# Kernel tuning notes

Hardware: AMD Instinct MI355X
Metric: run time of the kernel (lower is better)

The kernel has to match this reference:

```python
import jax, jax.numpy as jnp
import numpy as np

B, F, H, W = 1, 4, 20, 44
P = H * W            # 880 tokens per frame (20*44, from max_attention_size = 15*880)
S = F * P            # 3520 packed tokens
DIM, NH, FFN, OUT = 1536, 12, 6144, 64   # OUT = prod(patch_size)*out_dim = 4*16
HD = DIM // NH       # 128
C = HD // 2          # 64 rotary complex pairs
EPS = 1e-6


def _rope_angles():
    # Wan 3D RoPE: split C pairs as (C-2*(C//3), C//3, C//3) over (frame, h, w)
    cf, ch, cw = C - 2 * (C // 3), C // 3, C // 3
    def tab(n, cp):
        inv = 1.0 / (10000.0 ** (np.arange(cp) / cp))
        return np.outer(np.arange(n), inv)
    af = np.broadcast_to(tab(F, cf)[:, None, None, :], (F, H, W, cf))
    ah = np.broadcast_to(tab(H, ch)[None, :, None, :], (F, H, W, ch))
    aw = np.broadcast_to(tab(W, cw)[None, None, :, :], (F, H, W, cw))
    return np.concatenate([af, ah, aw], -1).reshape(S, C).astype(np.float32)


def setup_inputs() -> dict:
    key = jax.random.key(0)
    ks = jax.random.split(key, 24)
    g = lambda i, shape, s=0.02: jax.random.normal(ks[i], shape, dtype=jnp.float32) * s
    inp = {
        'x': jax.random.normal(ks[0], (B, S, DIM), dtype=jnp.float32),
        'e': g(1, (B, F, 6, DIM), 1.0),
        'e_head': g(2, (B, F, 2, DIM), 1.0),
        'rope_angles': jnp.asarray(_rope_angles()),
        'mod_block': g(3, (1, 6, DIM), 1.0 / float(np.sqrt(DIM))),
        'mod_head': g(4, (1, 2, DIM), 1.0 / float(np.sqrt(DIM))),
        'Wq': g(5, (DIM, DIM)), 'bq': jnp.zeros((DIM,), jnp.float32),
        'Wk': g(6, (DIM, DIM)), 'bk': jnp.zeros((DIM,), jnp.float32),
        'Wv': g(7, (DIM, DIM)), 'bv': jnp.zeros((DIM,), jnp.float32),
        'Wo': g(8, (DIM, DIM)), 'bo': jnp.zeros((DIM,), jnp.float32),
        'wq_norm': jnp.ones((DIM,), jnp.float32),
        'wk_norm': jnp.ones((DIM,), jnp.float32),
        'W1': g(9, (DIM, FFN)), 'b1': jnp.zeros((FFN,), jnp.float32),
        'W2': g(10, (FFN, DIM)), 'b2': jnp.zeros((DIM,), jnp.float32),
        'Wh': g(11, (DIM, OUT)), 'bh': jnp.zeros((OUT,), jnp.float32),
    }
    return inp


def _ln(x):
    # WanLayerNorm without elementwise affine
    m = jnp.mean(x, axis=-1, keepdims=True)
    v = jnp.var(x, axis=-1, keepdims=True)
    return (x - m) * jax.lax.rsqrt(v + EPS)


def _rms(x, w):
    return x * jax.lax.rsqrt(jnp.mean(x * x, axis=-1, keepdims=True) + EPS) * w


def _rope(t, ang):
    # t: [B,S,NH,HD]; adjacent pairs form complex numbers (view_as_complex style)
    tr = t.reshape(B, S, NH, C, 2)
    cos = jnp.cos(ang)[None, :, None, :]
    sin = jnp.sin(ang)[None, :, None, :]
    t0, t1 = tr[..., 0], tr[..., 1]
    return jnp.stack([t0 * cos - t1 * sin, t0 * sin + t1 * cos], -1).reshape(B, S, NH, HD)


def reference(x, e, e_head, rope_angles, mod_block, mod_head,
              Wq, bq, Wk, bk, Wv, bv, Wo, bo, wq_norm, wk_norm,
              W1, b1, W2, b2, Wh, bh):
    # ---- AdaLN modulation split (6-way) ----
    em = mod_block[:, None] + e                      # [B,F,6,DIM]
    e0, e1, e2, e3, e4, e5 = [em[:, :, i][:, :, None, :] for i in range(6)]

    xf = x.reshape(B, F, P, DIM)
    h = (_ln(xf) * (1 + e1) + e0).reshape(B, S, DIM)

    # ---- QK-RMSNorm + RoPE self attention (block-causal, block = one frame) ----
    q = _rope(_rms(h @ Wq + bq, wq_norm).reshape(B, S, NH, HD), rope_angles)
    k = _rope(_rms(h @ Wk + bk, wk_norm).reshape(B, S, NH, HD), rope_angles)
    v = (h @ Wv + bv).reshape(B, S, NH, HD)

    blk = jnp.arange(S) // P
    mask = blk[None, :] <= blk[:, None]              # [S,S] block-causal
    scores = jnp.einsum('bqhd,bkhd->bhqk', q, k) / np.float32(np.sqrt(HD))
    scores = jnp.where(mask[None, None], scores, jnp.float32(-1e30))
    attn = jax.nn.softmax(scores, axis=-1)
    y = jnp.einsum('bhqk,bkhd->bqhd', attn, v).reshape(B, S, DIM) @ Wo + bo

    xf = xf + y.reshape(B, F, P, DIM) * e2

    # ---- FFN with AdaLN modulation ----
    hf = (_ln(xf) * (1 + e4) + e3).reshape(B, S, DIM)
    ff = jax.nn.gelu(hf @ W1 + b1) @ W2 + b2
    xf = xf + ff.reshape(B, F, P, DIM) * e5

    # ---- OutputHead: modulated norm + linear ----
    eh = mod_head[:, None] + e_head                  # [B,F,2,DIM]
    eh0 = eh[:, :, 0][:, :, None, :]
    eh1 = eh[:, :, 1][:, :, None, :]
    out = (_ln(xf) * (1 + eh1) + eh0) @ Wh + bh      # [B,F,P,OUT]
    return out
```

## Files before the change

### kernel.cpp

```cpp
#include <hip/hip_runtime.h>
#include <cstdint>
#include <cstddef>

typedef __bf16 bf16;
typedef __bf16 bf16x2 __attribute__((ext_vector_type(2)));
typedef __bf16 bf16x4 __attribute__((ext_vector_type(4)));
typedef __bf16 bf16x8 __attribute__((ext_vector_type(8)));
typedef float f32x4 __attribute__((ext_vector_type(4)));
typedef unsigned int u32x4 __attribute__((ext_vector_type(4)));

#define S_TOK 3520
#define S_PAD 3584
#define P_TOK 880
#define NFRM 4
#define DIM 1536
#define NH 12
#define HD 128
#define FFN_D 6144
#define NOUT 64
#define EPSV 1e-6f
#define QSCALE 0.12751743f

__device__ __forceinline__ f32x4 mfma16(bf16x8 a, bf16x8 b, f32x4 c) {
  return __builtin_amdgcn_mfma_f32_16x16x32_bf16(a, b, c, 0, 0, 0);
}

__device__ __forceinline__ void gload_lds16(const bf16* g, bf16* l) {
  __builtin_amdgcn_global_load_lds(
      (const __attribute__((address_space(1))) unsigned int*)g,
      (__attribute__((address_space(3))) unsigned int*)l, 16, 0, 0);
}

__device__ __forceinline__ uint32_t pk2(float lo, float hi) {
  bf16x2 t;
  t[0] = (bf16)lo;
  t[1] = (bf16)hi;
  return __builtin_bit_cast(uint32_t, t);
}

__global__ __launch_bounds__(256) void k_prep(const float* __restrict__ e,
                                              const float* __restrict__ e_head,
                                              const float* __restrict__ mod_block,
                                              const float* __restrict__ mod_head,
                                              float* __restrict__ em,
                                              float* __restrict__ ehm) {
  int i = blockIdx.x * 256 + threadIdx.x;
  if (i < NFRM * 6 * DIM) em[i] = mod_block[i % (6 * DIM)] + e[i];
  int j = i - NFRM * 6 * DIM;
  if (j >= 0 && j < NFRM * 2 * DIM) ehm[j] = mod_head[j % (2 * DIM)] + e_head[j];
}

__global__ __launch_bounds__(256) void k_zero_vpad(bf16* __restrict__ vc) {
  size_t base = ((size_t)blockIdx.x * 28 + 27) * 4096 + 2048 + (size_t)threadIdx.x * 8;
#pragma unroll
  for (int i = 0; i < 8; ++i) vc[base + i] = (bf16)0.f;
}

__global__ __launch_bounds__(256) void k_transpose(const float* __restrict__ W,
                                                   bf16* __restrict__ Wt, int K, int N) {
  __shared__ float tile[32][33];
  int n0 = blockIdx.x * 32, k0 = blockIdx.y * 32;
  int tx = threadIdx.x & 31, ty = threadIdx.x >> 5;
#pragma unroll
  for (int j = 0; j < 4; ++j) {
    int k = k0 + ty * 4 + j;
    float v = (n0 + tx < N) ? W[(size_t)k * N + n0 + tx] : 0.f;
    tile[ty * 4 + j][tx] = v;
  }
  __syncthreads();
#pragma unroll
  for (int j = 0; j < 4; ++j) {
    int n = n0 + ty * 4 + j;
    if (n < N) Wt[(size_t)n * K + k0 + tx] = (bf16)tile[tx][ty * 4 + j];
  }
}

__global__ __launch_bounds__(256) void k_adaln(const float* __restrict__ in,
                                               bf16* __restrict__ out,
                                               const float* __restrict__ e_shift,
                                               const float* __restrict__ e_scale,
                                               int fstride) {
  int tok = blockIdx.x;
  int t = threadIdx.x;
  bf16* orow = out + (size_t)tok * DIM;
  if (tok >= S_TOK) {
#pragma unroll
    for (int i = 0; i < 6; ++i) orow[t * 6 + i] = (bf16)0.f;
    return;
  }
  const float* xrow = in + (size_t)tok * DIM;
  float v[6];
  float s = 0.f, sq = 0.f;
#pragma unroll
  for (int i = 0; i < 6; ++i) {
    v[i] = xrow[t * 6 + i];
    s += v[i];
    sq += v[i] * v[i];
  }
  for (int off = 32; off; off >>= 1) {
    s += __shfl_down(s, off);
    sq += __shfl_down(sq, off);
  }
  __shared__ float red[8];
  int wv = t >> 6, lane = t & 63;
  if (lane == 0) { red[wv] = s; red[4 + wv] = sq; }
  __syncthreads();
  float ts = red[0] + red[1] + red[2] + red[3];
  float tq = red[4] + red[5] + red[6] + red[7];
  float mean = ts * (1.f / DIM);
  float var = tq * (1.f / DIM) - mean * mean;
  float rstd = rsqrtf(var + EPSV);
  int f = tok / P_TOK;
  const float* sh = e_shift + (size_t)f * fstride;
  const float* sc = e_scale + (size_t)f * fstride;
#pragma unroll
  for (int i = 0; i < 6; ++i) {
    int d = t * 6 + i;
    orow[d] = (bf16)((v[i] - mean) * rstd * (1.f + sc[d]) + sh[d]);
  }
}

__global__ __launch_bounds__(256) void k_qkv_post(const bf16* __restrict__ qkv,
                                                  const float* __restrict__ wqn,
                                                  const float* __restrict__ wkn,
                                                  const float* __restrict__ ang,
                                                  bf16* __restrict__ qb,
                                                  bf16* __restrict__ kb,
                                                  bf16* __restrict__ vc) {
  int s = blockIdx.x;
  int t = threadIdx.x;
  const bf16* row = qkv + (size_t)s * 3 * DIM;
  float qv[6], kv[6], vv[6];
  float sqq = 0.f, sqk = 0.f;
  int d0 = t * 6;
#pragma unroll
  for (int i = 0; i < 6; ++i) {
    int d = d0 + i;
    qv[i] = (float)row[d];
    kv[i] = (float)row[DIM + d];
    vv[i] = (float)row[2 * DIM + d];
    sqq += qv[i] * qv[i];
    sqk += kv[i] * kv[i];
  }
  float a1 = sqq, a2 = sqk;
  for (int off = 32; off; off >>= 1) {
    a1 += __shfl_down(a1, off);
    a2 += __shfl_down(a2, off);
  }
  __shared__ float red[8];
  int wv = t >> 6, lane = t & 63;
  if (lane == 0) { red[wv] = a1; red[4 + wv] = a2; }
  __syncthreads();
  float tq = red[0] + red[1] + red[2] + red[3];
  float tk = red[4] + red[5] + red[6] + red[7];
  float rq = rsqrtf(tq * (1.f / DIM) + EPSV);
  float rk = rsqrtf(tk * (1.f / DIM) + EPSV);
#pragma unroll
  for (int p = 0; p < 3; ++p) {
    int d = d0 + p * 2;
    int h = d >> 7;
    int hd = d & 127;
    int c = hd >> 1;
    float a = ang[(size_t)s * 64 + c];
    float sa, ca;
    sincosf(a, &sa, &ca);
    float q0 = qv[p * 2] * rq * wqn[d], q1 = qv[p * 2 + 1] * rq * wqn[d + 1];
    float k0 = kv[p * 2] * rk * wkn[d], k1 = kv[p * 2 + 1] * rk * wkn[d + 1];
    size_t base = ((size_t)h * S_TOK + s) * HD + hd;
    qb[base]     = (bf16)((q0 * ca - q1 * sa) * QSCALE);
    qb[base + 1] = (bf16)((q0 * sa + q1 * ca) * QSCALE);
    kb[base]     = (bf16)(k0 * ca - k1 * sa);
    kb[base + 1] = (bf16)(k0 * sa + k1 * ca);
  }
  int f = s / P_TOK;
  int l = s - f * P_TOK;
  int lb = l >> 5, gg = (l >> 3) & 3, r = l & 7;
#pragma unroll
  for (int i = 0; i < 6; ++i) {
    int d = d0 + i;
    int h = d >> 7, hd = d & 127;
    vc[((((size_t)(h * NFRM + f)) * 28 + lb) * 512 + gg * 128 + hd) * 8 + r] = (bf16)vv[i];
  }
}

__global__ __launch_bounds__(320) void k_attn(const bf16* __restrict__ qb,
                                              const bf16* __restrict__ kb,
                                              const bf16* __restrict__ vc,
                                              bf16* __restrict__ parto,
                                              float* __restrict__ partml) {
  __shared__ __align__(16) bf16 Ks[2][512 * 8];
  __shared__ __align__(16) bf16 Vs[2][512 * 8];
  int h = blockIdx.x / 110;
  int p = blockIdx.x % 110;
  int f = (p < 11) ? 0 : (p < 33) ? 1 : (p < 66) ? 2 : 3;
  int cum = (f == 0) ? 0 : (f == 1) ? 11 : (f == 2) ? 33 : 66;
  int w = p - cum;
  int kc = w / 11;
  int qt = f * 11 + w % 11;
  int slot = blockIdx.x;
  int t = threadIdx.x;
  int wv = t >> 6, lane = t & 63;
  int r16 = lane & 15, g = lane >> 4;
  int q0 = qt * 80 + wv * 16;
  int kv0 = kc * P_TOK;
  const bf16* qbase = qb + ((size_t)h * S_TOK + q0 + r16) * HD + g * 8;
  bf16x8 qf[4];
#pragma unroll
  for (int kk = 0; kk < 4; ++kk) qf[kk] = *(const bf16x8*)(qbase + kk * 32);
  f32x4 acc[8] = {};
  float mrow = -1e30f, lrow = 0.f;
  int src01 = r16 + ((2 * g) & 3) * 16;
  int src23 = src01 + 16;
  bool glo = (g < 2);
  int sB = t + 256;
  int kr0 = t >> 4, kl0 = t & 15;
  int ks0 = (kl0 & 8) | ((kl0 ^ kr0) & 7);
  int kr1 = sB >> 4, kl1 = sB & 15;
  int ks1 = (kl1 & 8) | ((kl1 ^ kr1) & 7);
  const bf16* kh = kb + (size_t)h * S_TOK * HD;
  const bf16* vchunk = vc + ((size_t)(h * NFRM + kc)) * 28 * 4096;
#define STAGE_ATT(buf, jj)                                                  \
  do {                                                                      \
    int kvoj = (jj) * 32;                                                   \
    int gr0 = kv0 + kvoj + kr0; if (gr0 >= S_TOK) gr0 = 0;                  \
    int gr1 = kv0 + kvoj + kr1; if (gr1 >= S_TOK) gr1 = 0;                  \
    gload_lds16(kh + (size_t)gr0 * HD + ks0 * 8, Ks[buf] + t * 8);          \
    gload_lds16(kh + (size_t)gr1 * HD + ks1 * 8, Ks[buf] + sB * 8);         \
    gload_lds16(vchunk + (size_t)(jj) * 4096 + t * 8, Vs[buf] + t * 8);     \
    gload_lds16(vchunk + (size_t)(jj) * 4096 + sB * 8, Vs[buf] + sB * 8);   \
  } while (0)
  const int nsteps = (P_TOK + 31) >> 5;
  if (t < 256) STAGE_ATT(0, 0);
  int cur = 0;
  int vrb = g * 128 + r16;
  for (int j = 0; j < nsteps; ++j) {
    if (j + 1 < nsteps) {
      if (t < 256) STAGE_ATT(cur ^ 1, j + 1);
      asm volatile("s_waitcnt vmcnt(4)" ::: "memory");
    } else {
      asm volatile("s_waitcnt vmcnt(0)" ::: "memory");
    }
    __builtin_amdgcn_s_barrier();
    f32x4 st0 = {0.f, 0.f, 0.f, 0.f}, st1 = {0.f, 0.f, 0.f, 0.f};
#pragma unroll
    for (int kk = 0; kk < 4; ++kk) {
      int sl = g + 4 * kk;
      int ss = (sl & 8) | ((sl ^ r16) & 7);
      bf16x8 k0 = *(const bf16x8*)(Ks[cur] + (r16 * 16 + ss) * 8);
      bf16x8 k1 = *(const bf16x8*)(Ks[cur] + ((16 + r16) * 16 + ss) * 8);
      st0 = mfma16(k0, qf[kk], st0);
      st1 = mfma16(k1, qf[kk], st1);
    }
    float hm = (j == nsteps - 1) ? -1e30f : 0.f;
    float a0[4], a1[4];
#pragma unroll
    for (int r = 0; r < 4; ++r) {
      a0[r] = st0[r];
      a1[r] = st1[r] + hm;
    }
    float tm = fmaxf(fmaxf(fmaxf(a0[0], a0[1]), fmaxf(a0[2], a0[3])),
                     fmaxf(fmaxf(a1[0], a1[1]), fmaxf(a1[2], a1[3])));
    tm = fmaxf(tm, __shfl_xor(tm, 16));
    tm = fmaxf(tm, __shfl_xor(tm, 32));
    bool defer = __all(tm <= mrow + 8.f);
    if (!defer) {
      float mn = fmaxf(mrow, tm);
      float scl = exp2f(mrow - mn);
      lrow *= scl;
#pragma unroll
      for (int hb = 0; hb < 8; ++hb) {
        acc[hb][0] *= scl;
        acc[hb][1] *= scl;
        acc[hb][2] *= scl;
        acc[hb][3] *= scl;
      }
      mrow = mn;
    }
    float p0[4], p1[4], ps = 0.f;
#pragma unroll
    for (int r = 0; r < 4; ++r) {
      p0[r] = exp2f(a0[r] - mrow);
      p1[r] = exp2f(a1[r] - mrow);
      ps += p0[r] + p1[r];
    }
    lrow += ps;
    uint32_t A0 = pk2(p0[0], p0[1]), A1 = pk2(p0[2], p0[3]);
    uint32_t B0 = pk2(p1[0], p1[1]), B1 = pk2(p1[2], p1[3]);
    uint32_t sA0 = __shfl(A0, src01), sA1 = __shfl(A1, src01);
    uint32_t sB0 = __shfl(B0, src01), sB1 = __shfl(B1, src01);
    uint32_t tA0 = __shfl(A0, src23), tA1 = __shfl(A1, src23);
    uint32_t tB0 = __shfl(B0, src23), tB1 = __shfl(B1, src23);
    u32x4 wds;
    wds[0] = glo ? sA0 : sB0;
    wds[1] = glo ? sA1 : sB1;
    wds[2] = glo ? tA0 : tB0;
    wds[3] = glo ? tA1 : tB1;
    bf16x8 pb = __builtin_bit_cast(bf16x8, wds);
    const bf16* vsl = Vs[cur] + (size_t)vrb * 8;
#pragma unroll
    for (int hb = 0; hb < 8; ++hb) {
      bf16x8 vfr = *(const bf16x8*)(vsl + hb * 128);
      acc[hb] = mfma16(vfr, pb, acc[hb]);
    }
    asm volatile("" ::: "memory");
    __builtin_amdgcn_s_barrier();
    cur ^= 1;
  }
#undef STAGE_ATT
  lrow += __shfl_xor(lrow, 16);
  lrow += __shfl_xor(lrow, 32);
  bf16* obase = parto + ((size_t)slot * 5 + wv) * 2048;
#pragma unroll
  for (int hb = 0; hb < 8; ++hb) {
    bf16x4 ov;
    ov[0] = (bf16)acc[hb][0];
    ov[1] = (bf16)acc[hb][1];
    ov[2] = (bf16)acc[hb][2];
    ov[3] = (bf16)acc[hb][3];
    *(bf16x4*)(obase + (hb * 64 + lane) * 4) = ov;
  }
  if (g == 0) {
    float* mlb = partml + ((size_t)slot * 5 + wv) * 32;
    mlb[r16] = mrow;
    mlb[16 + r16] = lrow;
  }
}

__global__ __launch_bounds__(256) void k_att_reduce(const bf16* __restrict__ parto,
                                                    const float* __restrict__ partml,
                                                    bf16* __restrict__ attb) {
  int b = blockIdx.x;
  int h = b / 44, qt = b % 44;
  int f = qt / 11, j = qt % 11;
  int cum = (f == 0) ? 0 : (f == 1) ? 11 : (f == 2) ? 33 : 66;
  int t = threadIdx.x;
  int d = t & 127, half = t >> 7;
  int hb = d >> 4, g = (d >> 2) & 3, r = d & 3;
  int q0 = qt * 80;
  for (int it = 0; it < 40; ++it) {
    int qloc = it + 40 * half;
    int wv = qloc >> 4, r16 = qloc & 15;
    float m[4], l[4];
    float mt = -1e30f;
    for (int kc = 0; kc <= f; ++kc) {
      int slot = h * 110 + cum + kc * 11 + j;
      const float* mlb = partml + ((size_t)slot * 5 + wv) * 32;
      m[kc] = mlb[r16];
      l[kc] = mlb[16 + r16];
      mt = fmaxf(mt, m[kc]);
    }
    float lt = 0.f, o = 0.f;
    for (int kc = 0; kc <= f; ++kc) {
      int slot = h * 110 + cum + kc * 11 + j;
      float wgt = exp2f(m[kc] - mt);
      lt += l[kc] * wgt;
      o += (float)parto[(((size_t)slot * 5 + wv) * 8 + hb) * 256 + (g * 16 + r16) * 4 + r] * wgt;
    }
    attb[(size_t)(q0 + qloc) * DIM + h * HD + d] = (bf16)(o / lt);
  }
}

struct GemmP {
  const bf16* A;
  const bf16* Bt;
  int K;
  int Mtiles;
  int Ntiles;
  int Mreal;
  int mode;
  const float* bias0;
  const float* bias1;
  const float* bias2;
  const float* res;
  const float* emod;
  int e_fstride;
  float* outf;
  bf16* outb;
  int ldo;
};

__global__ __launch_bounds__(512, 4) void k_gemm(GemmP p) {
  int nwg = p.Mtiles * p.Ntiles;
  int bid = blockIdx.x;
  int xq = nwg >> 3, xr = nwg & 7;
  int xcd = bid & 7, jj = bid >> 3;
  int wg = (xcd < xr ? xcd * (xq + 1) : xr * (xq + 1) + (xcd - xr) * xq) + jj;
  int bm = wg % p.Mtiles;
  int bn = wg / p.Mtiles;
  __shared__ __align__(16) bf16 Asl[2][128 * 64];
  __shared__ __align__(16) bf16 Bsl[2][128 * 64];
  int t = threadIdx.x, lane = t & 63, wv = t >> 6;
  int r16 = lane & 15, g = lane >> 4;
  int s7 = r16 & 7;
  int wr = wv >> 2, wc = wv & 3;
  f32x4 acc[4][2] = {};
  const bf16* Ag = p.A + (size_t)bm * 128 * p.K;
  const bf16* Bg = p.Bt + (size_t)bn * 128 * p.K;
  int b0 = t, b1 = t + 512;
  int rw0 = b0 >> 3, cb0 = (b0 & 7) ^ (rw0 & 7);
  int rw1 = b1 >> 3, cb1 = (b1 & 7) ^ (rw1 & 7);
#define STAGE(d, kt)                                                          \
  do {                                                                        \
    int k0s = (kt) * 64;                                                      \
    gload_lds16(Ag + (size_t)rw0 * p.K + k0s + cb0 * 8, Asl[d] + b0 * 8);     \
    gload_lds16(Ag + (size_t)rw1 * p.K + k0s + cb1 * 8, Asl[d] + b1 * 8);     \
    gload_lds16(Bg + (size_t)rw0 * p.K + k0s + cb0 * 8, Bsl[d] + b0 * 8);     \
    gload_lds16(Bg + (size_t)rw1 * p.K + k0s + cb1 * 8, Bsl[d] + b1 * 8);     \
  } while (0)
  const int nt = p.K >> 6;
  STAGE(0, 0);
  int cur = 0;
  for (int tt = 0; tt < nt; ++tt) {
    if (tt + 1 < nt) {
      STAGE(cur ^ 1, tt + 1);
      asm volatile("s_waitcnt vmcnt(4)" ::: "memory");
    } else {
      asm volatile("s_waitcnt vmcnt(0)" ::: "memory");
    }
    __builtin_amdgcn_s_barrier();
    bf16x8 af[4][2], bfr[2][2];
#pragma unroll
    for (int mi = 0; mi < 4; ++mi)
#pragma unroll
      for (int kk = 0; kk < 2; ++kk)
        af[mi][kk] = *(const bf16x8*)(Asl[cur] + (size_t)(wr * 64 + mi * 16 + r16) * 64 +
                                      (((kk * 4 + g) ^ s7) * 8));
#pragma unroll
    for (int ni = 0; ni < 2; ++ni)
#pragma unroll
      for (int kk = 0; kk < 2; ++kk)
        bfr[ni][kk] = *(const bf16x8*)(Bsl[cur] + (size_t)(wc * 32 + ni * 16 + r16) * 64 +
                                       (((kk * 4 + g) ^ s7) * 8));
    __builtin_amdgcn_s_setprio(1);
#pragma unroll
    for (int mi = 0; mi < 4; ++mi)
#pragma unroll
      for (int ni = 0; ni < 2; ++ni)
#pragma unroll
        for (int kk = 0; kk < 2; ++kk)
          acc[mi][ni] = mfma16(af[mi][kk], bfr[ni][kk], acc[mi][ni]);
    __builtin_amdgcn_s_setprio(0);
    asm volatile("" ::: "memory");
    __builtin_amdgcn_s_barrier();
    cur ^= 1;
  }
#undef STAGE
  int mbase = bm * 128 + wr * 64, nbase = bn * 128 + wc * 32;
#pragma unroll
  for (int mi = 0; mi < 4; ++mi) {
#pragma unroll
    for (int ni = 0; ni < 2; ++ni) {
      int col = nbase + ni * 16 + r16;
#pragma unroll
      for (int r = 0; r < 4; ++r) {
        int row = mbase + mi * 16 + 4 * g + r;
        if (row >= p.Mreal) continue;
        float v = acc[mi][ni][r];
        if (p.mode == 0) {
          float b = col < DIM ? p.bias0[col]
                              : (col < 2 * DIM ? p.bias1[col - DIM] : p.bias2[col - 2 * DIM]);
          p.outb[(size_t)row * p.ldo + col] = (bf16)(v + b);
        } else if (p.mode == 1) {
          int fr = row / P_TOK;
          p.outf[(size_t)row * p.ldo + col] =
              p.res[(size_t)row * DIM + col] +
              (v + p.bias0[col]) * p.emod[(size_t)fr * p.e_fstride + col];
        } else if (p.mode == 2) {
          float xg = v + p.bias0[col];
          float gl = 0.5f * xg * (1.f + tanhf(0.7978845608028654f * (xg + 0.044715f * xg * xg * xg)));
          p.outb[(size_t)row * p.ldo + col] = (bf16)gl;
        } else {
          if (col < NOUT) p.outf[(size_t)row * p.ldo + col] = v + p.bias0[col];
        }
      }
    }
  }
}

extern "C" void kernel_launch(void* const* d_in, const int* in_sizes, int n_in,
                              void* d_out, int out_size, void* d_ws, size_t ws_size,
                              hipStream_t stream) {
  const float* x = (const float*)d_in[0];
  const float* e = (const float*)d_in[1];
  const float* e_head = (const float*)d_in[2];
  const float* ang = (const float*)d_in[3];
  const float* mod_block = (const float*)d_in[4];
  const float* mod_head = (const float*)d_in[5];
  const float* Wq = (const float*)d_in[6];
  const float* bq = (const float*)d_in[7];
  const float* Wk = (const float*)d_in[8];
  const float* bk = (const float*)d_in[9];
  const float* Wv = (const float*)d_in[10];
  const float* bv = (const float*)d_in[11];
  const float* Wo = (const float*)d_in[12];
  const float* bo = (const float*)d_in[13];
  const float* wqn = (const float*)d_in[14];
  const float* wkn = (const float*)d_in[15];
  const float* W1 = (const float*)d_in[16];
  const float* b1 = (const float*)d_in[17];
  const float* W2 = (const float*)d_in[18];
  const float* b2 = (const float*)d_in[19];
  const float* Wh = (const float*)d_in[20];
  const float* bh = (const float*)d_in[21];
  float* out = (float*)d_out;
  char* ws = (char*)d_ws;

  size_t WT_QKV = 0;
  size_t WT_O = WT_QKV + (size_t)3 * DIM * DIM * 2;
  size_t W1T = WT_O + (size_t)DIM * DIM * 2;
  size_t W2T = W1T + (size_t)FFN_D * DIM * 2;
  size_t WHT = W2T + (size_t)DIM * FFN_D * 2;
  size_t EMOFF = WHT + (size_t)128 * DIM * 2;
  size_t EHOFF = EMOFF + (size_t)NFRM * 6 * DIM * 4;
  size_t HB = EHOFF + (size_t)NFRM * 2 * DIM * 4;
  size_t CQKV = HB + (size_t)S_PAD * DIM * 2;
  size_t DQB = CQKV + (size_t)S_TOK * 3 * DIM * 4;
  size_t EATT = DQB + (size_t)3 * NH * S_TOK * HD * 2;
  size_t GXF2 = EATT + (size_t)S_PAD * DIM * 2;
  size_t END = GXF2 + (size_t)S_TOK * DIM * 4;
  if (ws_size < END) return;

  bf16* wtqkv = (bf16*)(ws + WT_QKV);
  bf16* wto = (bf16*)(ws + WT_O);
  bf16* w1t = (bf16*)(ws + W1T);
  bf16* w2t = (bf16*)(ws + W2T);
  bf16* wht = (bf16*)(ws + WHT);
  float* em = (float*)(ws + EMOFF);
  float* ehm = (float*)(ws + EHOFF);
  bf16* hb = (bf16*)(ws + HB);
  bf16* qkvb = (bf16*)(ws + CQKV);
  bf16* ffb = (bf16*)(ws + CQKV);
  bf16* parto = (bf16*)(ws + CQKV);
  float* partml = (float*)(ws + CQKV + (size_t)1320 * 5 * 2048 * 2);
  bf16* qbp = (bf16*)(ws + DQB);
  bf16* kbp = qbp + (size_t)NH * S_TOK * HD;
  bf16* vcp = kbp + (size_t)NH * S_TOK * HD;
  float* xf3 = (float*)(ws + DQB);
  bf16* attb = (bf16*)(ws + EATT);
  float* xf2 = (float*)(ws + GXF2);

  k_prep<<<(NFRM * 8 * DIM) / 256, 256, 0, stream>>>(e, e_head, mod_block, mod_head, em, ehm);
  k_zero_vpad<<<NH * NFRM, 256, 0, stream>>>(vcp);

  k_transpose<<<dim3(48, 48), 256, 0, stream>>>(Wq, wtqkv, DIM, DIM);
  k_transpose<<<dim3(48, 48), 256, 0, stream>>>(Wk, wtqkv + (size_t)DIM * DIM, DIM, DIM);
  k_transpose<<<dim3(48, 48), 256, 0, stream>>>(Wv, wtqkv + (size_t)2 * DIM * DIM, DIM, DIM);
  k_transpose<<<dim3(48, 48), 256, 0, stream>>>(Wo, wto, DIM, DIM);
  k_transpose<<<dim3(192, 48), 256, 0, stream>>>(W1, w1t, DIM, FFN_D);
  k_transpose<<<dim3(48, 192), 256, 0, stream>>>(W2, w2t, FFN_D, DIM);
  k_transpose<<<dim3(2, 48), 256, 0, stream>>>(Wh, wht, DIM, NOUT);
  hipMemsetAsync(ws + WHT + (size_t)NOUT * DIM * 2, 0, (size_t)(128 - NOUT) * DIM * 2, stream);
  hipMemsetAsync(ws + EATT + (size_t)S_TOK * DIM * 2, 0, (size_t)(S_PAD - S_TOK) * DIM * 2, stream);

  k_adaln<<<S_PAD, 256, 0, stream>>>(x, hb, em, em + DIM, 6 * DIM);

  GemmP g0{};
  g0.A = hb; g0.Bt = wtqkv; g0.K = DIM; g0.Mtiles = 28; g0.Ntiles = 36; g0.Mreal = S_TOK;
  g0.mode = 0; g0.bias0 = bq; g0.bias1 = bk; g0.bias2 = bv; g0.outb = qkvb; g0.ldo = 3 * DIM;
  k_gemm<<<28 * 36, 512, 0, stream>>>(g0);

  k_qkv_post<<<S_TOK, 256, 0, stream>>>(qkvb, wqn, wkn, ang, qbp, kbp, vcp);

  k_attn<<<NH * 110, 320, 0, stream>>>(qbp, kbp, vcp, parto, partml);
  k_att_reduce<<<NH * 44, 256, 0, stream>>>(parto, partml, attb);

  GemmP g1{};
  g1.A = attb; g1.Bt = wto; g1.K = DIM; g1.Mtiles = 28; g1.Ntiles = 12; g1.Mreal = S_TOK;
  g1.mode = 1; g1.bias0 = bo; g1.res = x; g1.emod = em + 2 * DIM; g1.e_fstride = 6 * DIM;
  g1.outf = xf2; g1.ldo = DIM;
  k_gemm<<<28 * 12, 512, 0, stream>>>(g1);

  k_adaln<<<S_PAD, 256, 0, stream>>>(xf2, hb, em + 3 * DIM, em + 4 * DIM, 6 * DIM);

  GemmP g2{};
  g2.A = hb; g2.Bt = w1t; g2.K = DIM; g2.Mtiles = 28; g2.Ntiles = 48; g2.Mreal = S_TOK;
  g2.mode = 2; g2.bias0 = b1; g2.outb = ffb; g2.ldo = FFN_D;
  k_gemm<<<28 * 48, 512, 0, stream>>>(g2);
  hipMemsetAsync(ws + CQKV + (size_t)S_TOK * FFN_D * 2, 0, (size_t)(S_PAD - S_TOK) * FFN_D * 2, stream);

  GemmP g3{};
  g3.A = ffb; g3.Bt = w2t; g3.K = FFN_D; g3.Mtiles = 28; g3.Ntiles = 12; g3.Mreal = S_TOK;
  g3.mode = 1; g3.bias0 = b2; g3.res = xf2; g3.emod = em + 5 * DIM; g3.e_fstride = 6 * DIM;
  g3.outf = xf3; g3.ldo = DIM;
  k_gemm<<<28 * 12, 512, 0, stream>>>(g3);

  k_adaln<<<S_PAD, 256, 0, stream>>>(xf3, hb, ehm, ehm + DIM, 2 * DIM);

  GemmP g4{};
  g4.A = hb; g4.Bt = wht; g4.K = DIM; g4.Mtiles = 28; g4.Ntiles = 1; g4.Mreal = S_TOK;
  g4.mode = 4; g4.bias0 = bh; g4.outf = out; g4.ldo = NOUT;
  k_gemm<<<28, 512, 0, stream>>>(g4);
}
```

Before: 656.6 us.

## Switch GEMM to BK=32 triple-buffered LDS pipeline with higher occupancy

```diff
diff --git a/kernel.cpp b/kernel.cpp
--- a/kernel.cpp
+++ b/kernel.cpp
@@ -379,7 +379,7 @@
   int ldo;
 };
 
-__global__ __launch_bounds__(512, 4) void k_gemm(GemmP p) {
+__global__ __launch_bounds__(512, 6) void k_gemm(GemmP p) {
   int nwg = p.Mtiles * p.Ntiles;
   int bid = blockIdx.x;
   int xq = nwg >> 3, xr = nwg & 7;
@@ -387,62 +387,59 @@
   int wg = (xcd < xr ? xcd * (xq + 1) : xr * (xq + 1) + (xcd - xr) * xq) + jj;
   int bm = wg % p.Mtiles;
   int bn = wg / p.Mtiles;
-  __shared__ __align__(16) bf16 Asl[2][128 * 64];
-  __shared__ __align__(16) bf16 Bsl[2][128 * 64];
+  __shared__ __align__(16) bf16 Asl[3][128 * 32];
+  __shared__ __align__(16) bf16 Bsl[3][128 * 32];
   int t = threadIdx.x, lane = t & 63, wv = t >> 6;
   int r16 = lane & 15, g = lane >> 4;
-  int s7 = r16 & 7;
   int wr = wv >> 2, wc = wv & 3;
   f32x4 acc[4][2] = {};
   const bf16* Ag = p.A + (size_t)bm * 128 * p.K;
   const bf16* Bg = p.Bt + (size_t)bn * 128 * p.K;
-  int b0 = t, b1 = t + 512;
-  int rw0 = b0 >> 3, cb0 = (b0 & 7) ^ (rw0 & 7);
-  int rw1 = b1 >> 3, cb1 = (b1 & 7) ^ (rw1 & 7);
+  int srow = t >> 2, sc = (t & 3) ^ (srow & 3);
 #define STAGE(d, kt)                                                          \
   do {                                                                        \
-    int k0s = (kt) * 64;                                                      \
-    gload_lds16(Ag + (size_t)rw0 * p.K + k0s + cb0 * 8, Asl[d] + b0 * 8);     \
-    gload_lds16(Ag + (size_t)rw1 * p.K + k0s + cb1 * 8, Asl[d] + b1 * 8);     \
-    gload_lds16(Bg + (size_t)rw0 * p.K + k0s + cb0 * 8, Bsl[d] + b0 * 8);     \
-    gload_lds16(Bg + (size_t)rw1 * p.K + k0s + cb1 * 8, Bsl[d] + b1 * 8);     \
+    int k0s = (kt) * 32;                                                      \
+    gload_lds16(Ag + (size_t)srow * p.K + k0s + sc * 8, Asl[d] + t * 8);      \
+    gload_lds16(Bg + (size_t)srow * p.K + k0s + sc * 8, Bsl[d] + t * 8);      \
   } while (0)
-  const int nt = p.K >> 6;
+  const int nt = p.K >> 5;
   STAGE(0, 0);
+  STAGE(1, 1);
   int cur = 0;
   for (int tt = 0; tt < nt; ++tt) {
-    if (tt + 1 < nt) {
-      STAGE(cur ^ 1, tt + 1);
+    int rem = nt - 1 - tt;
+    if (rem >= 2) {
+      int nb = cur + 2;
+      if (nb >= 3) nb -= 3;
+      STAGE(nb, tt + 2);
       asm volatile("s_waitcnt vmcnt(4)" ::: "memory");
+    } else if (rem == 1) {
+      asm volatile("s_waitcnt vmcnt(2)" ::: "memory");
     } else {
       asm volatile("s_waitcnt vmcnt(0)" ::: "memory");
     }
     __builtin_amdgcn_s_barrier();
-    bf16x8 af[4][2], bfr[2][2];
+    bf16x8 af[4], bfr[2];
+#pragma unroll
+    for (int mi = 0; mi < 4; ++mi) {
+      int row = wr * 64 + mi * 16 + r16;
+      af[mi] = *(const bf16x8*)(Asl[cur] + (size_t)(row * 4 + (g ^ (row & 3))) * 8);
+    }
+#pragma unroll
+    for (int ni = 0; ni < 2; ++ni) {
+      int row = wc * 32 + ni * 16 + r16;
+      bfr[ni] = *(const bf16x8*)(Bsl[cur] + (size_t)(row * 4 + (g ^ (row & 3))) * 8);
+    }
+    __builtin_amdgcn_s_setprio(1);
 #pragma unroll
     for (int mi = 0; mi < 4; ++mi)
 #pragma unroll
-      for (int kk = 0; kk < 2; ++kk)
-        af[mi][kk] = *(const bf16x8*)(Asl[cur] + (size_t)(wr * 64 + mi * 16 + r16) * 64 +
-                                      (((kk * 4 + g) ^ s7) * 8));
-#pragma unroll
-    for (int ni = 0; ni < 2; ++ni)
-#pragma unroll
-      for (int kk = 0; kk < 2; ++kk)
-        bfr[ni][kk] = *(const bf16x8*)(Bsl[cur] + (size_t)(wc * 32 + ni * 16 + r16) * 64 +
-                                       (((kk * 4 + g) ^ s7) * 8));
-    __builtin_amdgcn_s_setprio(1);
-#pragma unroll
-    for (int mi = 0; mi < 4; ++mi)
-#pragma unroll
       for (int ni = 0; ni < 2; ++ni)
-#pragma unroll
-        for (int kk = 0; kk < 2; ++kk)
-          acc[mi][ni] = mfma16(af[mi][kk], bfr[ni][kk], acc[mi][ni]);
+        acc[mi][ni] = mfma16(af[mi], bfr[ni], acc[mi][ni]);
     __builtin_amdgcn_s_setprio(0);
     asm volatile("" ::: "memory");
     __builtin_amdgcn_s_barrier();
-    cur ^= 1;
+    cur = (cur + 1 == 3) ? 0 : cur + 1;
   }
 #undef STAGE
   int mbase = bm * 128 + wr * 64, nbase = bn * 128 + wc * 32;
```

Result: slower. 723.0 us (+10.1%).
